# Optimization experiments

Hardware: AMD Instinct MI355X
Metric: run time of the kernel (lower is better)

The kernel has to match this reference:

```python
import jax, jax.numpy as jnp
import numpy as np

B, C_IN, N = 4, 64, 4096
E = 131072          # number of edges (avg degree 32)
C_OUT = 63          # out_channels - 1 because add_counts=True


def setup_inputs() -> dict:
    key = jax.random.key(0)
    k1, k2, k3, k4, k5 = jax.random.split(key, 5)
    x = jax.random.normal(k1, (B, C_IN, N), dtype=jnp.float32)
    adj_indices = jax.random.randint(k2, (2, E), 0, N, dtype=jnp.int64)
    adj_values = jax.random.uniform(k3, (E,), dtype=jnp.float32) * 12.0  # cart distances
    W = jax.random.normal(k4, (C_OUT, C_IN, 2), dtype=jnp.float32) * 0.05  # Conv1d weight (k=2)
    b = jax.random.normal(k5, (C_OUT,), dtype=jnp.float32) * 0.05
    return {"x": x, "adj_indices": adj_indices, "adj_values": adj_values, "W": W, "b": b}


def reference(x, adj_indices, adj_values, W, b):
    # Sparse equivalent of: adj_pw = expand_adjacency_tensor(adj).to_dense();
    # x @ adj_pw.T -> Conv1d(k=2, s=2) -> @ adj_pw[::2].
    n = x.shape[2]
    src = adj_indices[0]  # row 2k of adj_pw
    dst = adj_indices[1]  # row 2k+1 of adj_pw
    # Gather endpoint features: [B, C_in, E] each.
    xi = x[:, :, src]
    xj = x[:, :, dst]
    # Conv1d kernel=2 stride=2 over interleaved (src, dst) pairs == per-edge mix.
    out = (jnp.einsum('bce,oc->boe', xi, W[:, :, 0])
           + jnp.einsum('bce,oc->boe', xj, W[:, :, 1])
           + b[None, :, None])  # [B, C_out, E]
    # Scatter-add edge messages back to source nodes (adj_pw[::2]).
    y = jnp.zeros((x.shape[0], W.shape[0], n), dtype=x.dtype).at[:, :, src].add(out)
    # adj.to_dense().sum(dim=0): column sums of adjacency values.
    adj_sum = jax.ops.segment_sum(adj_values, dst, num_segments=n)  # [N]
    # normalize=True: divide by clamped column sums.
    denom = jnp.where(adj_sum == 0, jnp.ones_like(adj_sum), adj_sum)
    y = y / denom[None, None, :]
    # add_counts=True: append adj_sum as an extra channel.
    counts = jnp.broadcast_to(adj_sum[None, None, :], (x.shape[0], 1, n))
    return jnp.concatenate([y, counts], axis=1)  # [B, 64, N]
```

## Files before the change

kernel.cpp:

```cpp
#include <hip/hip_runtime.h>

#define BATCH   4
#define CIN     64
#define NNODES  4096
#define NEDGES  131072
#define COUT    63
#define NPB     16
#define CAP     128
#define GROUPS  16
#define GSHIFT  8
#define PBLK    128
#define SEGCAP  128
#define SEGSH   7

__global__ __launch_bounds__(1024) void k_prep(
    const float* __restrict__ x,
    const int* __restrict__ src,
    const int* __restrict__ dst,
    const float* __restrict__ vals,
    float* __restrict__ xT,
    int2* __restrict__ sgb,
    int2* __restrict__ dgb,
    int* __restrict__ scnt,
    int* __restrict__ dcnt)
{
    __shared__ float tile[64][65];
    __shared__ int2  sbuf[GROUPS][SEGCAP];
    __shared__ int2  dbuf[GROUPS][SEGCAP];
    __shared__ int   slcnt[GROUPS], dlcnt[GROUPS];

    const int blk = blockIdx.x;
    const int tid = threadIdx.x;
    const bool binner = blk < PBLK;

    if (binner && tid < GROUPS) { slcnt[tid] = 0; dlcnt[tid] = 0; }
    __syncthreads();

    if (binner) {
        int e = blk * 1024 + tid;
        int s = src[e], d = dst[e];
        float v = vals[e];
        int gs = s >> GSHIFT;
        int p = atomicAdd(&slcnt[gs], 1);
        if (p < SEGCAP) sbuf[gs][p] = make_int2(s, d);
        int gd = d >> GSHIFT;
        int q = atomicAdd(&dlcnt[gd], 1);
        if (q < SEGCAP) dbuf[gd][q] = make_int2(d, __float_as_int(v));
    }

    int b = blk >> 6;
    int n0 = (blk & 63) << 6;
    int tx = tid & 63, ty = tid >> 6;
    const float* xb = x + (size_t)b * CIN * NNODES;
#pragma unroll
    for (int c = ty; c < 64; c += 16)
        tile[c][tx] = xb[(size_t)c * NNODES + n0 + tx];
    __syncthreads();
#pragma unroll
    for (int n = ty; n < 64; n += 16)
        xT[((size_t)(n0 + n) * BATCH + b) * 64 + tx] = tile[tx][n];

    if (binner) {
        int g = tid >> 6, lane = tid & 63;
        int sc = min(slcnt[g], SEGCAP);
        int dc = min(dlcnt[g], SEGCAP);
        size_t base = ((size_t)(g * PBLK + blk)) << SEGSH;
        for (int k = lane; k < sc; k += 64) sgb[base + k] = sbuf[g][k];
        for (int k = lane; k < dc; k += 64) dgb[base + k] = dbuf[g][k];
        if (lane == 0) { scnt[g * PBLK + blk] = sc; dcnt[g * PBLK + blk] = dc; }
    }
}

__global__ __launch_bounds__(1024, 2) void k_main(
    const float* __restrict__ xT,
    const int2* __restrict__ sgb,
    const int2* __restrict__ dgb,
    const int* __restrict__ scnt,
    const int* __restrict__ dcnt,
    const float* __restrict__ W,
    const float* __restrict__ bias,
    float* __restrict__ out)
{
    __shared__ float w0s[64][65];
    __shared__ float w1s[64][65];
    __shared__ float aggs[NPB][260];
    __shared__ union U {
        int   lists[NPB][CAP];
        float res[BATCH][64][17];
    } u;
    __shared__ int   lcnt[NPB];
    __shared__ float adjs[NPB];
    __shared__ int   scn[PBLK], dcn[PBLK];

    const int tid   = threadIdx.x;
    const int nbase = blockIdx.x * NPB;
    const int g     = blockIdx.x >> 4;
    const int wv    = tid >> 6;
    const int lane  = tid & 63;
    const int n     = nbase + wv;

    if (tid < NPB) { lcnt[tid] = 0; adjs[tid] = 0.f; }
    if (tid < PBLK) {
        scn[tid] = scnt[g * PBLK + tid];
        dcn[tid] = dcnt[g * PBLK + tid];
    }
    {
        const float2* W2 = reinterpret_cast<const float2*>(W);
#pragma unroll
        for (int i = tid; i < COUT * CIN; i += 1024) {
            float2 v = W2[i];
            int o = i >> 6, c = i & 63;
            w0s[c][o] = v.x;
            w1s[c][o] = v.y;
        }
        if (tid < 64) { w0s[tid][63] = 0.f; w1s[tid][63] = 0.f; }
    }
    __syncthreads();

#pragma unroll 1
    for (int i = tid; i < PBLK * SEGCAP; i += 1024) {
        int seg = i >> SEGSH, k = i & (SEGCAP - 1);
        if (k < scn[seg]) {
            int2 e = sgb[(((size_t)g * PBLK + seg) << SEGSH) + k];
            unsigned a = (unsigned)(e.x - nbase);
            if (a < NPB) {
                int p = atomicAdd(&lcnt[a], 1);
                if (p < CAP) u.lists[a][p] = e.y;
            }
        }
    }
#pragma unroll 1
    for (int i = tid; i < PBLK * SEGCAP; i += 1024) {
        int seg = i >> SEGSH, k = i & (SEGCAP - 1);
        if (k < dcn[seg]) {
            int2 e = dgb[(((size_t)g * PBLK + seg) << SEGSH) + k];
            unsigned a = (unsigned)(e.x - nbase);
            if (a < NPB) atomicAdd(&adjs[a], __int_as_float(e.y));
        }
    }
    __syncthreads();

    const int cnt = lcnt[wv];
    {
        const int k1 = min(cnt, CAP);
        const int* L = u.lists[wv];
        const float* xb = xT + (size_t)lane * 4;
        float4 accA = make_float4(0.f, 0.f, 0.f, 0.f);
        float4 accB = make_float4(0.f, 0.f, 0.f, 0.f);
        int k = 0;
        for (; k + 8 <= k1; k += 8) {
            float4 v0 = *reinterpret_cast<const float4*>(xb + (size_t)L[k + 0] * 256);
            float4 v1 = *reinterpret_cast<const float4*>(xb + (size_t)L[k + 1] * 256);
            float4 v2 = *reinterpret_cast<const float4*>(xb + (size_t)L[k + 2] * 256);
            float4 v3 = *reinterpret_cast<const float4*>(xb + (size_t)L[k + 3] * 256);
            float4 v4 = *reinterpret_cast<const float4*>(xb + (size_t)L[k + 4] * 256);
            float4 v5 = *reinterpret_cast<const float4*>(xb + (size_t)L[k + 5] * 256);
            float4 v6 = *reinterpret_cast<const float4*>(xb + (size_t)L[k + 6] * 256);
            float4 v7 = *reinterpret_cast<const float4*>(xb + (size_t)L[k + 7] * 256);
            accA.x += (v0.x + v1.x) + (v2.x + v3.x);
            accA.y += (v0.y + v1.y) + (v2.y + v3.y);
            accA.z += (v0.z + v1.z) + (v2.z + v3.z);
            accA.w += (v0.w + v1.w) + (v2.w + v3.w);
            accB.x += (v4.x + v5.x) + (v6.x + v7.x);
            accB.y += (v4.y + v5.y) + (v6.y + v7.y);
            accB.z += (v4.z + v5.z) + (v6.z + v7.z);
            accB.w += (v4.w + v5.w) + (v6.w + v7.w);
        }
        for (; k < k1; ++k) {
            float4 v = *reinterpret_cast<const float4*>(xb + (size_t)L[k] * 256);
            accA.x += v.x; accA.y += v.y; accA.z += v.z; accA.w += v.w;
        }
        accA.x += accB.x; accA.y += accB.y; accA.z += accB.z; accA.w += accB.w;
        *reinterpret_cast<float4*>(&aggs[wv][lane * 4]) = accA;
    }
    __syncthreads();

    {
        int o = lane;
        float bval = (o < COUT) ? bias[o] : 0.f;
        const float* xrow = xT + (size_t)n * 256;

        float acc0[4] = {0.f, 0.f, 0.f, 0.f};
        float acc1[4] = {0.f, 0.f, 0.f, 0.f};

#pragma unroll 1
        for (int c4 = 0; c4 < 64; c4 += 4) {
            float w00 = w0s[c4 + 0][o], w01 = w0s[c4 + 1][o];
            float w02 = w0s[c4 + 2][o], w03 = w0s[c4 + 3][o];
            float w10 = w1s[c4 + 0][o], w11 = w1s[c4 + 1][o];
            float w12 = w1s[c4 + 2][o], w13 = w1s[c4 + 3][o];
#pragma unroll
            for (int b = 0; b < 4; ++b) {
                float4 xv = *reinterpret_cast<const float4*>(xrow + b * 64 + c4);
                float4 av = *reinterpret_cast<const float4*>(&aggs[wv][b * 64 + c4]);
                acc0[b] += w00 * xv.x + w01 * xv.y + w02 * xv.z + w03 * xv.w;
                acc1[b] += w10 * av.x + w11 * av.y + w12 * av.z + w13 * av.w;
            }
        }

        float dg = (float)cnt;
        float aj = adjs[wv];
        float rd = 1.f / ((aj == 0.f) ? 1.f : aj);
#pragma unroll
        for (int b = 0; b < 4; ++b) {
            float v = (o < COUT) ? (dg * (acc0[b] + bval) + acc1[b]) * rd : aj;
            u.res[b][o][wv] = v;
        }
    }
    __syncthreads();

#pragma unroll
    for (int i = tid; i < BATCH * 64 * NPB; i += 1024) {
        int b = i >> 10, o = (i >> 4) & 63, nl = i & 15;
        out[((size_t)(b * 64 + o)) * NNODES + nbase + nl] = u.res[b][o][nl];
    }
}

extern "C" void kernel_launch(void* const* d_in, const int* in_sizes, int n_in,
                              void* d_out, int out_size, void* d_ws, size_t ws_size,
                              hipStream_t stream) {
    const float* x    = (const float*)d_in[0];
    const int*   adj  = (const int*)d_in[1];
    const float* vals = (const float*)d_in[2];
    const float* W    = (const float*)d_in[3];
    const float* bias = (const float*)d_in[4];
    float* out = (float*)d_out;

    const int* src = adj;
    const int* dst = adj + NEDGES;

    char* ws = (char*)d_ws;
    float* xT   = (float*)(ws);
    int2*  sgb  = (int2*) (ws + (4 << 20));
    int2*  dgb  = (int2*) (ws + (6 << 20));
    int*   scnt = (int*)  (ws + (8 << 20));
    int*   dcnt = (int*)  (ws + (8 << 20) + (8 << 10));

    k_prep<<<BATCH * (NNODES / 64), 1024, 0, stream>>>(x, src, dst, vals,
                                                       xT, sgb, dgb, scnt, dcnt);
    k_main<<<NNODES / NPB, 1024, 0, stream>>>(xT, sgb, dgb, scnt, dcnt,
                                              W, bias, out);
}
```

Measured before the change: 44.29 us.

## Bin edges per 16-node block so main kernel scans only its own buckets

Edge binning now uses 256 groups of 16 nodes, one per main-kernel block, spread across all 256 prep blocks at 512 edges each. Each main block therefore reads only its own edges instead of filtering a 256-node group's worth, which cuts wasted global reads and compare work. Source entries are packed into one int holding the local node and neighbor index, halving that buffer. Per-bucket capacity drops to 16, so the risk is silent overflow if a node block receives more than 16 edges from one prep block.

```diff
diff --git a/kernel.cpp b/kernel.cpp
--- a/kernel.cpp
+++ b/kernel.cpp
@@ -7,11 +7,11 @@
 #define COUT    63
 #define NPB     16
 #define CAP     128
-#define GROUPS  16
-#define GSHIFT  8
-#define PBLK    128
-#define SEGCAP  128
-#define SEGSH   7
+#define GROUPS  256
+#define GSHIFT  4
+#define PBLK    256
+#define SEGCAP  16
+#define SEGSH   4
 
 __global__ __launch_bounds__(1024) void k_prep(
     const float* __restrict__ x,
@@ -19,33 +19,60 @@
     const int* __restrict__ dst,
     const float* __restrict__ vals,
     float* __restrict__ xT,
-    int2* __restrict__ sgb,
+    int* __restrict__ sgb,
     int2* __restrict__ dgb,
     int* __restrict__ scnt,
     int* __restrict__ dcnt)
 {
     __shared__ float tile[64][65];
-    __shared__ int2  sbuf[GROUPS][SEGCAP];
-    __shared__ int2  dbuf[GROUPS][SEGCAP];
-    __shared__ int   slcnt[GROUPS], dlcnt[GROUPS];
+    __shared__ union BB {
+        int  s[GROUPS][SEGCAP];
+        int2 d[GROUPS][SEGCAP];
+    } bb;
+    __shared__ int bcnt[GROUPS];
 
     const int blk = blockIdx.x;
     const int tid = threadIdx.x;
-    const bool binner = blk < PBLK;
-
-    if (binner && tid < GROUPS) { slcnt[tid] = 0; dlcnt[tid] = 0; }
-    __syncthreads();
-
-    if (binner) {
-        int e = blk * 1024 + tid;
-        int s = src[e], d = dst[e];
-        float v = vals[e];
-        int gs = s >> GSHIFT;
-        int p = atomicAdd(&slcnt[gs], 1);
-        if (p < SEGCAP) sbuf[gs][p] = make_int2(s, d);
-        int gd = d >> GSHIFT;
-        int q = atomicAdd(&dlcnt[gd], 1);
-        if (q < SEGCAP) dbuf[gd][q] = make_int2(d, __float_as_int(v));
+    const int w = tid >> 6, lane = tid & 63;
+
+    int s_ = 0, d_ = 0; float v_ = 0.f;
+    const bool hasE = tid < 512;
+    if (hasE) {
+        int e = blk * 512 + tid;
+        s_ = src[e]; d_ = dst[e]; v_ = vals[e];
+    }
+
+    if (tid < GROUPS) bcnt[tid] = 0;
+    __syncthreads();
+    if (hasE) {
+        int g = s_ >> GSHIFT;
+        int p = atomicAdd(&bcnt[g], 1);
+        if (p < SEGCAP) bb.s[g][p] = ((s_ & (NPB - 1)) << 12) | d_;
+    }
+    __syncthreads();
+#pragma unroll
+    for (int it = 0; it < GROUPS / 16; ++it) {
+        int g = w * 16 + it;
+        int sc = min(bcnt[g], SEGCAP);
+        if (lane < sc) sgb[((size_t)(g * PBLK + blk) << SEGSH) + lane] = bb.s[g][lane];
+        if (lane == 0) scnt[g * PBLK + blk] = sc;
+    }
+    __syncthreads();
+
+    if (tid < GROUPS) bcnt[tid] = 0;
+    __syncthreads();
+    if (hasE) {
+        int g = d_ >> GSHIFT;
+        int q = atomicAdd(&bcnt[g], 1);
+        if (q < SEGCAP) bb.d[g][q] = make_int2(d_ & (NPB - 1), __float_as_int(v_));
+    }
+    __syncthreads();
+#pragma unroll
+    for (int it = 0; it < GROUPS / 16; ++it) {
+        int g = w * 16 + it;
+        int dc = min(bcnt[g], SEGCAP);
+        if (lane < dc) dgb[((size_t)(g * PBLK + blk) << SEGSH) + lane] = bb.d[g][lane];
+        if (lane == 0) dcnt[g * PBLK + blk] = dc;
     }
 
     int b = blk >> 6;
@@ -59,21 +86,11 @@
 #pragma unroll
     for (int n = ty; n < 64; n += 16)
         xT[((size_t)(n0 + n) * BATCH + b) * 64 + tx] = tile[tx][n];
-
-    if (binner) {
-        int g = tid >> 6, lane = tid & 63;
-        int sc = min(slcnt[g], SEGCAP);
-        int dc = min(dlcnt[g], SEGCAP);
-        size_t base = ((size_t)(g * PBLK + blk)) << SEGSH;
-        for (int k = lane; k < sc; k += 64) sgb[base + k] = sbuf[g][k];
-        for (int k = lane; k < dc; k += 64) dgb[base + k] = dbuf[g][k];
-        if (lane == 0) { scnt[g * PBLK + blk] = sc; dcnt[g * PBLK + blk] = dc; }
-    }
 }
 
 __global__ __launch_bounds__(1024, 2) void k_main(
     const float* __restrict__ xT,
-    const int2* __restrict__ sgb,
+    const int* __restrict__ sgb,
     const int2* __restrict__ dgb,
     const int* __restrict__ scnt,
     const int* __restrict__ dcnt,
@@ -93,8 +110,8 @@
     __shared__ int   scn[PBLK], dcn[PBLK];
 
     const int tid   = threadIdx.x;
-    const int nbase = blockIdx.x * NPB;
-    const int g     = blockIdx.x >> 4;
+    const int g     = blockIdx.x;
+    const int nbase = g * NPB;
     const int wv    = tid >> 6;
     const int lane  = tid & 63;
     const int n     = nbase + wv;
@@ -121,21 +138,18 @@
     for (int i = tid; i < PBLK * SEGCAP; i += 1024) {
         int seg = i >> SEGSH, k = i & (SEGCAP - 1);
         if (k < scn[seg]) {
-            int2 e = sgb[(((size_t)g * PBLK + seg) << SEGSH) + k];
-            unsigned a = (unsigned)(e.x - nbase);
-            if (a < NPB) {
-                int p = atomicAdd(&lcnt[a], 1);
-                if (p < CAP) u.lists[a][p] = e.y;
-            }
+            int e = sgb[((size_t)g * PBLK << SEGSH) + i];
+            int a = e >> 12;
+            int p = atomicAdd(&lcnt[a], 1);
+            if (p < CAP) u.lists[a][p] = e & 0xFFF;
         }
     }
 #pragma unroll 1
     for (int i = tid; i < PBLK * SEGCAP; i += 1024) {
         int seg = i >> SEGSH, k = i & (SEGCAP - 1);
         if (k < dcn[seg]) {
-            int2 e = dgb[(((size_t)g * PBLK + seg) << SEGSH) + k];
-            unsigned a = (unsigned)(e.x - nbase);
-            if (a < NPB) atomicAdd(&adjs[a], __int_as_float(e.y));
+            int2 e = dgb[((size_t)g * PBLK << SEGSH) + i];
+            atomicAdd(&adjs[e.x], __int_as_float(e.y));
         }
     }
     __syncthreads();
@@ -231,10 +245,10 @@
 
     char* ws = (char*)d_ws;
     float* xT   = (float*)(ws);
-    int2*  sgb  = (int2*) (ws + (4 << 20));
-    int2*  dgb  = (int2*) (ws + (6 << 20));
-    int*   scnt = (int*)  (ws + (8 << 20));
-    int*   dcnt = (int*)  (ws + (8 << 20) + (8 << 10));
+    int*   sgb  = (int*)  (ws + (4 << 20));
+    int2*  dgb  = (int2*) (ws + (8 << 20));
+    int*   scnt = (int*)  (ws + (16 << 20));
+    int*   dcnt = (int*)  (ws + (16 << 20) + (256 << 10));
 
     k_prep<<<BATCH * (NNODES / 64), 1024, 0, stream>>>(x, src, dst, vals,
                                                        xT, sgb, dgb, scnt, dcnt);
```

After: 39.08 us. 1.13x faster.
